# Performance work log

Measured on AMD Instinct MI355X. Metric: run time of the kernel, lower is better.

## Reference

```python
import jax, jax.numpy as jnp
import numpy as np

K, D, N = 256, 1000, 65536


def setup_inputs() -> dict:
    key = jax.random.key(0)
    k1, k2 = jax.random.split(key)
    encoder_embedding = jax.random.normal(k1, (N, D), dtype=jnp.float32)
    # matches torch init: uniform_(-1/K, 1/D)
    weight = jax.random.uniform(k2, (K, D), dtype=jnp.float32, minval=-1.0 / K, maxval=1.0 / D)
    return {"encoder_embedding": encoder_embedding, "weight": weight}


def reference(encoder_embedding, weight):
    # squared L2 distance via expansion (same math as sum((x[:,None]-w)**2, -1)
    # without materializing the (N,K,D) broadcast intermediate)
    x_sq = jnp.sum(encoder_embedding * encoder_embedding, axis=1, keepdims=True)  # (N,1)
    w_sq = jnp.sum(weight * weight, axis=1)                                       # (K,)
    cross = encoder_embedding @ weight.T                                          # (N,K)
    distance = x_sq - 2.0 * cross + w_sq                                          # (N,K)
    idx = jnp.argmin(distance, axis=1)                                            # (N,)
    return weight[idx]                                                            # (N,D)
```

## Files before the change

### kernel.cpp

```cpp
#include <hip/hip_runtime.h>
#include <stdint.h>

#define N_ROWS 65536
#define DIM    1000
#define KCB    256

#define RB     64
#define DT     32
#define PITCH  36

__global__ __launch_bounds__(256) void wsq_old_kernel(const float* __restrict__ w,
                                                      float* __restrict__ wsq) {
    const int wave = threadIdx.x >> 6;
    const int lane = threadIdx.x & 63;
    const int k = blockIdx.x * 4 + wave;
    double s = 0.0;
    for (int c = lane; c < DIM / 4; c += 64) {
        const float4 v = *(const float4*)(w + k * DIM + c * 4);
        s += (double)v.x * v.x + (double)v.y * v.y + (double)v.z * v.z + (double)v.w * v.w;
    }
    #pragma unroll
    for (int off = 32; off; off >>= 1) s += __shfl_down(s, off, 64);
    if (lane == 0) wsq[k] = (float)s;
}

__global__ __launch_bounds__(256) void xsq_old_kernel(const float* __restrict__ x,
                                                      float* __restrict__ xsq) {
    const int wave = threadIdx.x >> 6;
    const int lane = threadIdx.x & 63;
    const int row = blockIdx.x * 4 + wave;
    double s = 0.0;
    for (int c = lane; c < DIM / 4; c += 64) {
        const float4 v = *(const float4*)(x + (size_t)row * DIM + c * 4);
        s += (double)v.x * v.x + (double)v.y * v.y + (double)v.z * v.z + (double)v.w * v.w;
    }
    #pragma unroll
    for (int off = 32; off; off >>= 1) s += __shfl_down(s, off, 64);
    if (lane == 0) xsq[row] = (float)s;
}

__global__ __launch_bounds__(256) void vq_old_kernel(const float* __restrict__ x,
                                                     const float* __restrict__ w,
                                                     const float* __restrict__ wsq,
                                                     const float* __restrict__ xsq,
                                                     float* __restrict__ out) {
    __shared__ float Xs[RB * PITCH];
    __shared__ float Ws[KCB * PITCH];
    __shared__ int   lidx[RB];

    const int tid  = threadIdx.x;
    const int row0 = blockIdx.x * RB;
    const int kt = tid & 31;
    const int rt = tid >> 5;

    double acc[8][8];
    #pragma unroll
    for (int i = 0; i < 8; i++)
        #pragma unroll
        for (int j = 0; j < 8; j++) acc[i][j] = 0.0;

    const int wk = tid >> 3;
    const int wg = tid & 7;
    const int xr = tid >> 2;
    const int xg = tid & 3;

    for (int d0 = 0; d0 < DIM; d0 += DT) {
        #pragma unroll
        for (int p = 0; p < 8; p++) {
            const int k = p * 32 + wk;
            const int d = d0 + wg * 4;
            float4 v = make_float4(0.f, 0.f, 0.f, 0.f);
            if (d < DIM) v = *(const float4*)(w + k * DIM + d);
            *(float4*)(&Ws[k * PITCH + wg * 4]) = v;
        }
        #pragma unroll
        for (int p = 0; p < 2; p++) {
            const int off = (xg + p * 4) * 4;
            const int d = d0 + off;
            float4 v = make_float4(0.f, 0.f, 0.f, 0.f);
            if (d < DIM) v = *(const float4*)(x + (size_t)(row0 + xr) * DIM + d);
            *(float4*)(&Xs[xr * PITCH + off]) = v;
        }
        __syncthreads();

        #pragma unroll
        for (int dq = 0; dq < DT; dq += 4) {
            float4 xf[8], wf[8];
            #pragma unroll
            for (int i = 0; i < 8; i++)
                xf[i] = *(const float4*)(&Xs[(rt + 8 * i) * PITCH + dq]);
            #pragma unroll
            for (int j = 0; j < 8; j++)
                wf[j] = *(const float4*)(&Ws[(kt + 32 * j) * PITCH + dq]);
            #pragma unroll
            for (int i = 0; i < 8; i++)
                #pragma unroll
                for (int j = 0; j < 8; j++) {
                    float p = xf[i].x * wf[j].x;
                    p = fmaf(xf[i].y, wf[j].y, p);
                    p = fmaf(xf[i].z, wf[j].z, p);
                    p = fmaf(xf[i].w, wf[j].w, p);
                    acc[i][j] += (double)p;
                }
        }
        __syncthreads();
    }

    #pragma unroll
    for (int i = 0; i < 8; i++) {
        const float xs = xsq[row0 + rt + 8 * i];
        float bestv = 3.4e38f;
        int   bestk = 0;
        #pragma unroll
        for (int j = 0; j < 8; j++) {
            const int k = kt + 32 * j;
            const float c32 = (float)acc[i][j];
            const float t1  = xs - 2.0f * c32;
            const float s   = t1 + wsq[k];
            if (s < bestv || (s == bestv && k < bestk)) { bestv = s; bestk = k; }
        }
        #pragma unroll
        for (int m = 16; m >= 1; m >>= 1) {
            const float ov = __shfl_xor(bestv, m, 64);
            const int   ok = __shfl_xor(bestk, m, 64);
            if (ov < bestv || (ov == bestv && ok < bestk)) { bestv = ov; bestk = ok; }
        }
        if (kt == 0) lidx[rt + 8 * i] = bestk;
    }
    __syncthreads();

    const int wave = tid >> 6;
    const int lane = tid & 63;
    for (int r = wave; r < RB; r += 4) {
        const int k = lidx[r];
        const float4* src = (const float4*)(w + k * DIM);
        float4* dst = (float4*)(out + (size_t)(row0 + r) * DIM);
        for (int c = lane; c < DIM / 4; c += 64) dst[c] = src[c];
    }
}


#define RBM    64
#define NSTEP  32
#define XHI    0
#define XLO    4096
#define WHIO   8192
#define WLOO   24576
#define LDSB   40960

typedef short bf16x8 __attribute__((ext_vector_type(8)));
typedef float f32x4  __attribute__((ext_vector_type(4)));
typedef unsigned short us8 __attribute__((ext_vector_type(8)));

__device__ __forceinline__ unsigned short f2bf(float f) {
    union { float f; unsigned int u; } v; v.f = f;
    return (unsigned short)((v.u + 0x7FFFu + ((v.u >> 16) & 1u)) >> 16);
}
__device__ __forceinline__ float bf2f(unsigned short h) {
    union { float f; unsigned int u; } v; v.u = ((unsigned int)h) << 16;
    return v.f;
}
__device__ __forceinline__ void glds16(const void* g, void* l) {
    __builtin_amdgcn_global_load_lds((const __attribute__((address_space(1))) unsigned int*)g,
                                     (__attribute__((address_space(3))) unsigned int*)l, 16, 0, 0);
}

__global__ __launch_bounds__(256) void prep_kernel(const float* __restrict__ w,
        float* __restrict__ wsq, unsigned short* __restrict__ whi, unsigned short* __restrict__ wlo) {
    const int wave = threadIdx.x >> 6;
    const int lane = threadIdx.x & 63;
    const int k = blockIdx.x * 4 + wave;
    double s = 0.0;
    for (int c = lane; c < DIM / 4; c += 64) {
        const float4 v = *(const float4*)(w + k * DIM + c * 4);
        s += (double)v.x * v.x + (double)v.y * v.y + (double)v.z * v.z + (double)v.w * v.w;
    }
    #pragma unroll
    for (int off = 32; off; off >>= 1) s += __shfl_down(s, off, 64);
    if (lane == 0) wsq[k] = (float)s;

    const int ct = k >> 4, kl = k & 15;
    for (int c = lane; c < 256; c += 64) {
        float4 v = make_float4(0.f, 0.f, 0.f, 0.f);
        if (c < DIM / 4) v = *(const float4*)(w + k * DIM + c * 4);
        ushort4 h, l;
        h.x = f2bf(v.x); l.x = f2bf(v.x - bf2f(h.x));
        h.y = f2bf(v.y); l.y = f2bf(v.y - bf2f(h.y));
        h.z = f2bf(v.z); l.z = f2bf(v.z - bf2f(h.z));
        h.w = f2bf(v.w); l.w = f2bf(v.w - bf2f(h.w));
        const int step = c >> 3, qq = c & 7;
        const int pos = step * 16384 + ct * 1024 + ((qq >> 1) * 16 + kl) * 16 + (qq & 1) * 8;
        *(ushort4*)((char*)whi + pos) = h;
        *(ushort4*)((char*)wlo + pos) = l;
    }
}

__global__ __launch_bounds__(256) void xsq_s1_kernel(const float* __restrict__ x,
        float* __restrict__ xsq, float* __restrict__ s1) {
    const int wave = threadIdx.x >> 6;
    const int lane = threadIdx.x & 63;
    const int row = blockIdx.x * 4 + wave;
    double s = 0.0, a = 0.0;
    for (int c = lane; c < DIM / 4; c += 64) {
        const float4 v = *(const float4*)(x + (size_t)row * DIM + c * 4);
        s += (double)v.x * v.x + (double)v.y * v.y + (double)v.z * v.z + (double)v.w * v.w;
        a += (double)fabsf(v.x) + (double)fabsf(v.y) + (double)fabsf(v.z) + (double)fabsf(v.w);
    }
    #pragma unroll
    for (int off = 32; off; off >>= 1) { s += __shfl_down(s, off, 64); a += __shfl_down(a, off, 64); }
    if (lane == 0) { xsq[row] = (float)s; s1[row] = (float)a; }
}

__global__ __launch_bounds__(256, 2) void vq_main_kernel(
        const float* __restrict__ x, const float* __restrict__ w,
        const float* __restrict__ wsq, const float* __restrict__ xsq,
        const float* __restrict__ s1,
        const unsigned short* __restrict__ whi, const unsigned short* __restrict__ wlo,
        float* __restrict__ out) {
    __shared__ __align__(16) char lds[2 * LDSB];
    const int tid  = threadIdx.x;
    const int lane = tid & 63;
    const int wv   = tid >> 6;
    const int row0 = blockIdx.x * RBM;

    const int qp   = (lane >> 4) & 3;
    const int srow = wv * 16 + (lane & 15);
    const size_t xrow_off = (size_t)(row0 + srow) * DIM;
    const int xpos0 = wv * 1024 + lane * 16;

    f32x4 accm[4][4], accc[4][4];
    {
        const f32x4 z = {0.f, 0.f, 0.f, 0.f};
        #pragma unroll
        for (int i = 0; i < 4; i++)
            #pragma unroll
            for (int j = 0; j < 4; j++) { accm[i][j] = z; accc[i][j] = z; }
    }

    float4 xa0, xb0, xa1, xb1;
    auto xloadA = [&](int t) {
        const int dA = t * 32 + qp * 8, dB = dA + 4;
        xa0 = (dA <= DIM - 4) ? *(const float4*)(x + xrow_off + dA) : make_float4(0.f, 0.f, 0.f, 0.f);
        xb0 = (dB <= DIM - 4) ? *(const float4*)(x + xrow_off + dB) : make_float4(0.f, 0.f, 0.f, 0.f);
    };
    auto xloadB = [&](int t) {
        const int dA = t * 32 + qp * 8, dB = dA + 4;
        xa1 = (dA <= DIM - 4) ? *(const float4*)(x + xrow_off + dA) : make_float4(0.f, 0.f, 0.f, 0.f);
        xb1 = (dB <= DIM - 4) ? *(const float4*)(x + xrow_off + dB) : make_float4(0.f, 0.f, 0.f, 0.f);
    };
    auto xstore = [&](int b, const float4& xa, const float4& xb) {
        us8 h, l;
        h[0] = f2bf(xa.x); l[0] = f2bf(xa.x - bf2f(h[0]));
        h[1] = f2bf(xa.y); l[1] = f2bf(xa.y - bf2f(h[1]));
        h[2] = f2bf(xa.z); l[2] = f2bf(xa.z - bf2f(h[2]));
        h[3] = f2bf(xa.w); l[3] = f2bf(xa.w - bf2f(h[3]));
        h[4] = f2bf(xb.x); l[4] = f2bf(xb.x - bf2f(h[4]));
        h[5] = f2bf(xb.y); l[5] = f2bf(xb.y - bf2f(h[5]));
        h[6] = f2bf(xb.z); l[6] = f2bf(xb.z - bf2f(h[6]));
        h[7] = f2bf(xb.w); l[7] = f2bf(xb.w - bf2f(h[7]));
        *(us8*)(lds + b * LDSB + XHI + xpos0) = h;
        *(us8*)(lds + b * LDSB + XLO + xpos0) = l;
    };
    auto wstage = [&](int b, int t) {
        #pragma unroll
        for (int i = 0; i < 4; i++) {
            const int ch = wv * 4 + i;
            glds16(whi + (size_t)t * 8192 + ch * 512 + lane * 8, lds + b * LDSB + WHIO + ch * 1024);
            glds16(wlo + (size_t)t * 8192 + ch * 512 + lane * 8, lds + b * LDSB + WLOO + ch * 1024);
        }
    };
    auto compute = [&](int b) {
        const char* base = lds + b * LDSB;
        bf16x8 ahi[4], alo[4];
        #pragma unroll
        for (int rt = 0; rt < 4; rt++) {
            ahi[rt] = *(const bf16x8*)(base + XHI + rt * 1024 + lane * 16);
            alo[rt] = *(const bf16x8*)(base + XLO + rt * 1024 + lane * 16);
        }
        __builtin_amdgcn_s_setprio(1);
        #pragma unroll
        for (int jt = 0; jt < 4; jt++) {
            const int ct = wv * 4 + jt;
            const bf16x8 bhi = *(const bf16x8*)(base + WHIO + ct * 1024 + lane * 16);
            const bf16x8 blo = *(const bf16x8*)(base + WLOO + ct * 1024 + lane * 16);
            #pragma unroll
            for (int rt = 0; rt < 4; rt++) {
                accm[rt][jt] = __builtin_amdgcn_mfma_f32_16x16x32_bf16(ahi[rt], bhi, accm[rt][jt], 0, 0, 0);
                accc[rt][jt] = __builtin_amdgcn_mfma_f32_16x16x32_bf16(ahi[rt], blo, accc[rt][jt], 0, 0, 0);
                accc[rt][jt] = __builtin_amdgcn_mfma_f32_16x16x32_bf16(alo[rt], bhi, accc[rt][jt], 0, 0, 0);
            }
        }
        __builtin_amdgcn_s_setprio(0);
    };

    wstage(0, 0);
    xloadA(0); xstore(0, xa0, xb0);
    xloadB(1);
    __syncthreads();

    for (int t = 0; t < 30; t += 2) {
        xloadA(t + 2);
        xstore(1 - (t & 1), xa1, xb1);
        wstage(1 - (t & 1), t + 1);
        compute(t & 1);
        __syncthreads();
        xloadB(t + 3);
        xstore(t & 1, xa0, xb0);
        wstage(t & 1, t + 2);
        compute(1 - (t & 1));
        __syncthreads();
    }
    xstore(1, xa1, xb1);
    wstage(1, 31);
    compute(0);
    __syncthreads();
    compute(1);
    __syncthreads();

    #pragma unroll
    for (int i = 0; i < 4; i++)
        #pragma unroll
        for (int j = 0; j < 4; j++) accm[i][j] += accc[i][j];

    const int g  = lane >> 4;
    const int cl = lane & 15;
    float* minw = (float*)lds;
    unsigned short* m16 = (unsigned short*)(lds + 1024);
    int* lidx   = (int*)(lds + 3072);
    int* mlist  = (int*)(lds + 3328);
    int* nmulti = (int*)(lds + 3584);

    float wsqv[4];
    #pragma unroll
    for (int jt = 0; jt < 4; jt++) wsqv[jt] = wsq[wv * 64 + jt * 16 + cl];

    float xsv[4][4], mv[4][4];
    #pragma unroll
    for (int rt = 0; rt < 4; rt++)
        #pragma unroll
        for (int e = 0; e < 4; e++) {
            const int r = row0 + rt * 16 + g * 4 + e;
            const float xs = xsq[r];
            xsv[rt][e] = xs;
            mv[rt][e] = 2.5e-6f * s1[r] + 6e-7f * (xs + 64.0f) + 1e-12f;
        }

    #pragma unroll
    for (int rt = 0; rt < 4; rt++)
        #pragma unroll
        for (int jt = 0; jt < 4; jt++)
            #pragma unroll
            for (int e = 0; e < 4; e++) {
                const float c = accm[rt][jt][e];
                const float t1 = xsv[rt][e] - 2.0f * c;
                accm[rt][jt][e] = t1 + wsqv[jt];
            }

    #pragma unroll
    for (int rt = 0; rt < 4; rt++)
        #pragma unroll
        for (int e = 0; e < 4; e++) {
            float mn = fminf(fminf(accm[rt][0][e], accm[rt][1][e]), fminf(accm[rt][2][e], accm[rt][3][e]));
            #pragma unroll
            for (int m = 8; m; m >>= 1) mn = fminf(mn, __shfl_xor(mn, m, 64));
            if (cl == 0) minw[(rt * 16 + g * 4 + e) * 4 + wv] = mn;
        }
    __syncthreads();

    float tv[4][4];
    #pragma unroll
    for (int rt = 0; rt < 4; rt++)
        #pragma unroll
        for (int e = 0; e < 4; e++) {
            const int r = rt * 16 + g * 4 + e;
            const float gm = fminf(fminf(minw[r * 4 + 0], minw[r * 4 + 1]),
                                   fminf(minw[r * 4 + 2], minw[r * 4 + 3]));
            tv[rt][e] = gm + mv[rt][e];
        }
    #pragma unroll
    for (int rt = 0; rt < 4; rt++)
        #pragma unroll
        for (int jt = 0; jt < 4; jt++)
            #pragma unroll
            for (int e = 0; e < 4; e++) {
                const unsigned long long b = __ballot(accm[rt][jt][e] <= tv[rt][e]);
                if (cl == 0)
                    m16[(rt * 16 + g * 4 + e) * 16 + wv * 4 + jt] = (unsigned short)(b >> (g * 16));
            }
    __syncthreads();

    if (wv == 0) {
        unsigned int mw[8];
        int cnt = 0;
        #pragma unroll
        for (int i = 0; i < 8; i++) {
            mw[i] = (unsigned int)m16[lane * 16 + 2 * i] | ((unsigned int)m16[lane * 16 + 2 * i + 1] << 16);
            cnt += __popc(mw[i]);
        }
        int kb = 0;
        #pragma unroll
        for (int i = 7; i >= 0; i--) if (mw[i]) kb = 32 * i + __ffs(mw[i]) - 1;
        lidx[lane] = kb;
        const unsigned long long act = __ballot(cnt > 1);
        if (cnt > 1) {
            const int pfx = __popcll(act & ((1ull << lane) - 1ull));
            mlist[pfx] = lane;
        }
        if (lane == 0) nmulti[0] = __popcll(act);
    }
    __syncthreads();

    const int nm = nmulti[0];
    for (int i = wv; i < nm; i += 4) {
        const int r = mlist[i];
        unsigned int mw[8];
        #pragma unroll
        for (int q = 0; q < 8; q++)
            mw[q] = (unsigned int)m16[r * 16 + 2 * q] | ((unsigned int)m16[r * 16 + 2 * q + 1] << 16);

        float4 xq[4];
        #pragma unroll
        for (int p = 0; p < 4; p++) {
            const int c = lane + 64 * p;
            xq[p] = (c < DIM / 4) ? *(const float4*)(x + (size_t)(row0 + r) * DIM + c * 4)
                                  : make_float4(0.f, 0.f, 0.f, 0.f);
        }
        const float xs = xsq[row0 + r];
        float bv = 3.4e38f; int bk = KCB;
        for (int wd = 0; wd < 8; wd++) {
            unsigned int m = mw[wd];
            while (m) {
                const int k = wd * 32 + __ffs(m) - 1;
                m &= m - 1;
                double a = 0.0;
                #pragma unroll
                for (int p = 0; p < 4; p++) {
                    const int c = lane + 64 * p;
                    if (c < DIM / 4) {
                        const float4 wq = *(const float4*)(w + (size_t)k * DIM + c * 4);
                        float pt = xq[p].x * wq.x;
                        pt = fmaf(xq[p].y, wq.y, pt);
                        pt = fmaf(xq[p].z, wq.z, pt);
                        pt = fmaf(xq[p].w, wq.w, pt);
                        a += (double)pt;
                    }
                }
                #pragma unroll
                for (int off = 32; off; off >>= 1) a += __shfl_xor(a, off, 64);
                const float c32 = (float)a;
                const float t1 = xs - 2.0f * c32;
                const float sv = t1 + wsq[k];
                if (sv < bv) { bv = sv; bk = k; }
            }
        }
        if (lane == 0) lidx[r] = bk;
    }
    __syncthreads();

    for (int r = wv; r < RBM; r += 4) {
        const int k = lidx[r];
        const float4* src = (const float4*)(w + (size_t)k * DIM);
        float4* dst = (float4*)(out + (size_t)(row0 + r) * DIM);
        for (int c = lane; c < DIM / 4; c += 64) dst[c] = src[c];
    }
}

extern "C" void kernel_launch(void* const* d_in, const int* in_sizes, int n_in,
                              void* d_out, int out_size, void* d_ws, size_t ws_size,
                              hipStream_t stream) {
    const float* x = (const float*)d_in[0];
    const float* w = (const float*)d_in[1];
    float* out  = (float*)d_out;
    float* base = (float*)d_ws;

    const size_t NEED = 393472ull * 4ull;
    if (ws_size < NEED) {
        float* wsq = base;
        float* xsq = wsq + KCB;
        wsq_old_kernel<<<KCB / 4, 256, 0, stream>>>(w, wsq);
        xsq_old_kernel<<<N_ROWS / 4, 256, 0, stream>>>(x, xsq);
        vq_old_kernel<<<N_ROWS / RB, 256, 0, stream>>>(x, w, wsq, xsq, out);
        return;
    }

    float*          wsq = base;
    float*          xsq = base + 256;
    float*          s1  = base + 65792;
    unsigned short* whi = (unsigned short*)(base + 131328);
    unsigned short* wlo = (unsigned short*)(base + 262400);

    prep_kernel<<<KCB / 4, 256, 0, stream>>>(w, wsq, whi, wlo);
    xsq_s1_kernel<<<N_ROWS / 4, 256, 0, stream>>>(x, xsq, s1);
    vq_main_kernel<<<N_ROWS / RBM, 256, 0, stream>>>(x, w, wsq, xsq, s1, whi, wlo, out);
}
```

Before: 572.1 us.

## Replace full barriers with counted vmcnt waits to overlap W staging with MFMA

Reworks the double-buffered main loop so each iteration issues the next x global load, waits only on the specific outstanding memory operations with hand-counted s_waitcnt vmcnt values, computes on one buffer, and then stores x and issues async W global_load_lds into the other. Full __syncthreads is replaced by a bare s_barrier plus explicit lgkmcnt waits. The goal is to keep global-to-LDS W transfers in flight during MFMA compute instead of draining all memory at every barrier. The x loads also become branchless, using clamped addresses and zeroing afterwards. The hand-tuned wait counts are fragile: if they don't match the real number of issued loads, the kernel can read stale LDS data.

```diff
diff --git a/kernel.cpp b/kernel.cpp
--- a/kernel.cpp
+++ b/kernel.cpp
@@ -151,6 +151,10 @@
 typedef short bf16x8 __attribute__((ext_vector_type(8)));
 typedef float f32x4  __attribute__((ext_vector_type(4)));
 typedef unsigned short us8 __attribute__((ext_vector_type(8)));
+
+#define SBAR()  __builtin_amdgcn_s_barrier()
+#define WAITV(n) asm volatile("s_waitcnt vmcnt(" #n ")" ::: "memory")
+#define WAITL()  asm volatile("s_waitcnt lgkmcnt(0)" ::: "memory")
 
 __device__ __forceinline__ unsigned short f2bf(float f) {
     union { float f; unsigned int u; } v; v.f = f;
@@ -239,14 +243,22 @@
 
     float4 xa0, xb0, xa1, xb1;
     auto xloadA = [&](int t) {
-        const int dA = t * 32 + qp * 8, dB = dA + 4;
-        xa0 = (dA <= DIM - 4) ? *(const float4*)(x + xrow_off + dA) : make_float4(0.f, 0.f, 0.f, 0.f);
-        xb0 = (dB <= DIM - 4) ? *(const float4*)(x + xrow_off + dB) : make_float4(0.f, 0.f, 0.f, 0.f);
+        const int dA = t * 32 + qp * 8;
+        const int pA = dA > 992 ? 992 : dA;
+        const int pB = dA + 4 > 996 ? 996 : dA + 4;
+        xa0 = *(const float4*)(x + xrow_off + pA);
+        xb0 = *(const float4*)(x + xrow_off + pB);
+        if (dA > 992)     xa0 = make_float4(0.f, 0.f, 0.f, 0.f);
+        if (dA + 4 > 996) xb0 = make_float4(0.f, 0.f, 0.f, 0.f);
     };
     auto xloadB = [&](int t) {
-        const int dA = t * 32 + qp * 8, dB = dA + 4;
-        xa1 = (dA <= DIM - 4) ? *(const float4*)(x + xrow_off + dA) : make_float4(0.f, 0.f, 0.f, 0.f);
-        xb1 = (dB <= DIM - 4) ? *(const float4*)(x + xrow_off + dB) : make_float4(0.f, 0.f, 0.f, 0.f);
+        const int dA = t * 32 + qp * 8;
+        const int pA = dA > 992 ? 992 : dA;
+        const int pB = dA + 4 > 996 ? 996 : dA + 4;
+        xa1 = *(const float4*)(x + xrow_off + pA);
+        xb1 = *(const float4*)(x + xrow_off + pB);
+        if (dA > 992)     xa1 = make_float4(0.f, 0.f, 0.f, 0.f);
+        if (dA + 4 > 996) xb1 = make_float4(0.f, 0.f, 0.f, 0.f);
     };
     auto xstore = [&](int b, const float4& xa, const float4& xb) {
         us8 h, l;
@@ -294,28 +306,38 @@
     };
 
     wstage(0, 0);
-    xloadA(0); xstore(0, xa0, xb0);
+    xloadA(0);
+    xstore(0, xa0, xb0);
     xloadB(1);
-    __syncthreads();
+    wstage(1, 1);
+    WAITL(); SBAR();
 
     for (int t = 0; t < 30; t += 2) {
         xloadA(t + 2);
-        xstore(1 - (t & 1), xa1, xb1);
-        wstage(1 - (t & 1), t + 1);
-        compute(t & 1);
-        __syncthreads();
+        WAITV(12);
+        compute(0);
+        WAITV(10);
+        xstore(1, xa1, xb1);
+        WAITL();
+        wstage(0, t + 2);
+        SBAR();
         xloadB(t + 3);
-        xstore(t & 1, xa0, xb0);
-        wstage(t & 1, t + 2);
-        compute(1 - (t & 1));
-        __syncthreads();
-    }
+        WAITV(12);
+        compute(1);
+        WAITV(10);
+        xstore(0, xa0, xb0);
+        WAITL();
+        wstage(1, t + 3);
+        SBAR();
+    }
+    WAITV(10);
+    compute(0);
+    WAITV(8);
     xstore(1, xa1, xb1);
-    wstage(1, 31);
-    compute(0);
-    __syncthreads();
+    WAITL();
+    SBAR();
+    WAITV(0);
     compute(1);
-    __syncthreads();
 
     #pragma unroll
     for (int i = 0; i < 4; i++)
```

New measurement: 579.9 us. No clear change (+1.4%).

## Merge accumulators, load W-lo to registers, shrink LDS for 3 blocks/CU

Applied to the files above, without the earlier changes.

The separate main and correction accumulators are merged into one set, halving accumulator registers. The low-part W tiles now go directly from global memory into registers instead of through LDS, which shrinks each LDS buffer from 40 KB to 24 KB. Launch bounds rise to 3 blocks per CU. The pipeline becomes a single-step loop with clamped, branch-free x loads. In exchange, the W-lo global loads are no longer staged asynchronously and may add latency inside compute, and the merged accumulators change rounding slightly.

```diff
diff --git a/kernel.cpp b/kernel.cpp
--- a/kernel.cpp
+++ b/kernel.cpp
@@ -145,8 +145,7 @@
 #define XHI    0
 #define XLO    4096
 #define WHIO   8192
-#define WLOO   24576
-#define LDSB   40960
+#define LDSB   24576
 
 typedef short bf16x8 __attribute__((ext_vector_type(8)));
 typedef float f32x4  __attribute__((ext_vector_type(4)));
@@ -211,7 +210,7 @@
     if (lane == 0) { xsq[row] = (float)s; s1[row] = (float)a; }
 }
 
-__global__ __launch_bounds__(256, 2) void vq_main_kernel(
+__global__ __launch_bounds__(256, 3) void vq_main_kernel(
         const float* __restrict__ x, const float* __restrict__ w,
         const float* __restrict__ wsq, const float* __restrict__ xsq,
         const float* __restrict__ s1,
@@ -228,27 +227,27 @@
     const size_t xrow_off = (size_t)(row0 + srow) * DIM;
     const int xpos0 = wv * 1024 + lane * 16;
 
-    f32x4 accm[4][4], accc[4][4];
+    f32x4 acc[4][4];
     {
         const f32x4 z = {0.f, 0.f, 0.f, 0.f};
         #pragma unroll
         for (int i = 0; i < 4; i++)
             #pragma unroll
-            for (int j = 0; j < 4; j++) { accm[i][j] = z; accc[i][j] = z; }
-    }
-
-    float4 xa0, xb0, xa1, xb1;
-    auto xloadA = [&](int t) {
-        const int dA = t * 32 + qp * 8, dB = dA + 4;
-        xa0 = (dA <= DIM - 4) ? *(const float4*)(x + xrow_off + dA) : make_float4(0.f, 0.f, 0.f, 0.f);
-        xb0 = (dB <= DIM - 4) ? *(const float4*)(x + xrow_off + dB) : make_float4(0.f, 0.f, 0.f, 0.f);
+            for (int j = 0; j < 4; j++) acc[i][j] = z;
+    }
+    bf16x8 blo[4];
+    float4 xa, xb;
+
+    auto xload = [&](int t) {
+        const int dA = (t & 31) * 32 + qp * 8;
+        const int pA = dA > 992 ? 992 : dA;
+        const int pB = dA + 4 > 996 ? 996 : dA + 4;
+        xa = *(const float4*)(x + xrow_off + pA);
+        xb = *(const float4*)(x + xrow_off + pB);
+        if (dA > 992)     xa = make_float4(0.f, 0.f, 0.f, 0.f);
+        if (dA + 4 > 996) xb = make_float4(0.f, 0.f, 0.f, 0.f);
     };
-    auto xloadB = [&](int t) {
-        const int dA = t * 32 + qp * 8, dB = dA + 4;
-        xa1 = (dA <= DIM - 4) ? *(const float4*)(x + xrow_off + dA) : make_float4(0.f, 0.f, 0.f, 0.f);
-        xb1 = (dB <= DIM - 4) ? *(const float4*)(x + xrow_off + dB) : make_float4(0.f, 0.f, 0.f, 0.f);
-    };
-    auto xstore = [&](int b, const float4& xa, const float4& xb) {
+    auto xstore = [&](int b) {
         us8 h, l;
         h[0] = f2bf(xa.x); l[0] = f2bf(xa.x - bf2f(h[0]));
         h[1] = f2bf(xa.y); l[1] = f2bf(xa.y - bf2f(h[1]));
@@ -266,10 +265,14 @@
         for (int i = 0; i < 4; i++) {
             const int ch = wv * 4 + i;
             glds16(whi + (size_t)t * 8192 + ch * 512 + lane * 8, lds + b * LDSB + WHIO + ch * 1024);
-            glds16(wlo + (size_t)t * 8192 + ch * 512 + lane * 8, lds + b * LDSB + WLOO + ch * 1024);
         }
     };
-    auto compute = [&](int b) {
+    auto bloLoad = [&](int t) {
+        #pragma unroll
+        for (int i = 0; i < 4; i++)
+            blo[i] = *(const bf16x8*)(wlo + (size_t)t * 8192 + (wv * 4 + i) * 512 + lane * 8);
+    };
+    auto computeT = [&](int b) {
         const char* base = lds + b * LDSB;
         bf16x8 ahi[4], alo[4];
         #pragma unroll
@@ -280,47 +283,33 @@
         __builtin_amdgcn_s_setprio(1);
         #pragma unroll
         for (int jt = 0; jt < 4; jt++) {
-            const int ct = wv * 4 + jt;
-            const bf16x8 bhi = *(const bf16x8*)(base + WHIO + ct * 1024 + lane * 16);
-            const bf16x8 blo = *(const bf16x8*)(base + WLOO + ct * 1024 + lane * 16);
+            const bf16x8 bhi = *(const bf16x8*)(base + WHIO + (wv * 4 + jt) * 1024 + lane * 16);
             #pragma unroll
             for (int rt = 0; rt < 4; rt++) {
-                accm[rt][jt] = __builtin_amdgcn_mfma_f32_16x16x32_bf16(ahi[rt], bhi, accm[rt][jt], 0, 0, 0);
-                accc[rt][jt] = __builtin_amdgcn_mfma_f32_16x16x32_bf16(ahi[rt], blo, accc[rt][jt], 0, 0, 0);
-                accc[rt][jt] = __builtin_amdgcn_mfma_f32_16x16x32_bf16(alo[rt], bhi, accc[rt][jt], 0, 0, 0);
+                acc[rt][jt] = __builtin_amdgcn_mfma_f32_16x16x32_bf16(ahi[rt], bhi,     acc[rt][jt], 0, 0, 0);
+                acc[rt][jt] = __builtin_amdgcn_mfma_f32_16x16x32_bf16(ahi[rt], blo[jt], acc[rt][jt], 0, 0, 0);
+                acc[rt][jt] = __builtin_amdgcn_mfma_f32_16x16x32_bf16(alo[rt], bhi,     acc[rt][jt], 0, 0, 0);
             }
         }
         __builtin_amdgcn_s_setprio(0);
     };
 
+    xload(0); xstore(0);
     wstage(0, 0);
-    xloadA(0); xstore(0, xa0, xb0);
-    xloadB(1);
-    __syncthreads();
-
-    for (int t = 0; t < 30; t += 2) {
-        xloadA(t + 2);
-        xstore(1 - (t & 1), xa1, xb1);
-        wstage(1 - (t & 1), t + 1);
-        compute(t & 1);
+    __syncthreads();
+
+    for (int t = 0; t < 31; t++) {
+        const int cur = t & 1;
+        bloLoad(t);
+        xload(t + 1);
+        wstage(1 - cur, t + 1);
+        computeT(cur);
+        xstore(1 - cur);
         __syncthreads();
-        xloadB(t + 3);
-        xstore(t & 1, xa0, xb0);
-        wstage(t & 1, t + 2);
-        compute(1 - (t & 1));
-        __syncthreads();
-    }
-    xstore(1, xa1, xb1);
-    wstage(1, 31);
-    compute(0);
-    __syncthreads();
-    compute(1);
-    __syncthreads();
-
-    #pragma unroll
-    for (int i = 0; i < 4; i++)
-        #pragma unroll
-        for (int j = 0; j < 4; j++) accm[i][j] += accc[i][j];
+    }
+    bloLoad(31);
+    computeT(1);
+    __syncthreads();
 
     const int g  = lane >> 4;
     const int cl = lane & 15;
@@ -351,16 +340,16 @@
         for (int jt = 0; jt < 4; jt++)
             #pragma unroll
             for (int e = 0; e < 4; e++) {
-                const float c = accm[rt][jt][e];
+                const float c = acc[rt][jt][e];
                 const float t1 = xsv[rt][e] - 2.0f * c;
-                accm[rt][jt][e] = t1 + wsqv[jt];
+                acc[rt][jt][e] = t1 + wsqv[jt];
             }
 
     #pragma unroll
     for (int rt = 0; rt < 4; rt++)
         #pragma unroll
         for (int e = 0; e < 4; e++) {
-            float mn = fminf(fminf(accm[rt][0][e], accm[rt][1][e]), fminf(accm[rt][2][e], accm[rt][3][e]));
+            float mn = fminf(fminf(acc[rt][0][e], acc[rt][1][e]), fminf(acc[rt][2][e], acc[rt][3][e]));
             #pragma unroll
             for (int m = 8; m; m >>= 1) mn = fminf(mn, __shfl_xor(mn, m, 64));
             if (cl == 0) minw[(rt * 16 + g * 4 + e) * 4 + wv] = mn;
@@ -383,7 +372,7 @@
         for (int jt = 0; jt < 4; jt++)
             #pragma unroll
             for (int e = 0; e < 4; e++) {
-                const unsigned long long b = __ballot(accm[rt][jt][e] <= tv[rt][e]);
+                const unsigned long long b = __ballot(acc[rt][jt][e] <= tv[rt][e]);
                 if (cl == 0)
                     m16[(rt * 16 + g * 4 + e) * 16 + wv * 4 + jt] = (unsigned short)(b >> (g * 16));
             }
```

Result: slower. 606.1 us (+5.9%).
